# Optimization experiments

Hardware: AMD Instinct MI355X
Metric: run time of the kernel (lower is better)

## Reference

```python
import jax, jax.numpy as jnp
import numpy as np

HEADS = 8
DHEAD = 64
A_SCALE = 8.0  # cosine-attention logit scale (a=8 in source)
ROPE_BASE = 10000.0


def _mp_weight(w, centered):
    # Magnitude-preserving (EDM2-style) weight: optional zero-mean over fan-in,
    # unit-norm per output row, scaled by 1/sqrt(fan_in).
    if centered:
        w = w - w.mean(axis=1, keepdims=True)
    w = w / (jnp.linalg.norm(w, axis=1, keepdims=True) + 1e-8)
    return w / jnp.sqrt(jnp.asarray(w.shape[1], w.dtype))


def _rope_cos_sin(Hs, Ws, d, dtype=jnp.float32):
    # 2D axial RoPE: first d/4 rotation pairs encode row position, last d/4 column position.
    quarter = d // 4
    freqs = 1.0 / (ROPE_BASE ** (jnp.arange(quarter, dtype=dtype) / quarter))  # [d/4]
    ah = jnp.arange(Hs, dtype=dtype)[:, None] * freqs                          # [H, d/4]
    aw = jnp.arange(Ws, dtype=dtype)[:, None] * freqs                          # [W, d/4]
    ang = jnp.concatenate([
        jnp.broadcast_to(ah[:, None, :], (Hs, Ws, quarter)),
        jnp.broadcast_to(aw[None, :, :], (Hs, Ws, quarter)),
    ], axis=-1).reshape(Hs * Ws, d // 2)                                       # [L, d/2]
    return jnp.cos(ang), jnp.sin(ang)


def _apply_rope(t, cos, sin):
    # t: [N, h, L, d]; rotate interleaved pairs.
    x1, x2 = t[..., 0::2], t[..., 1::2]
    r1 = x1 * cos - x2 * sin
    r2 = x1 * sin + x2 * cos
    return jnp.stack([r1, r2], axis=-1).reshape(t.shape)


def setup_inputs() -> dict:
    key = jax.random.key(0)
    ks = jax.random.split(key, 8)
    N, C, Hs, Ws = 8, 256, 32, 32
    E, Hc = 512, 512
    return {
        "x": jax.random.normal(ks[0], (N, C, Hs, Ws), jnp.float32),
        "w": jax.random.normal(ks[1], (N, E), jnp.float32),
        "InputGain": jax.random.uniform(ks[2], (3 * Hc,), jnp.float32),
        "ResidualGain": jax.random.uniform(ks[3], (C,), jnp.float32),
        "qkv_w": jax.random.normal(ks[4], (3 * Hc, C), jnp.float32),
        "qkv_b": jnp.zeros((3 * Hc,), jnp.float32),
        "mod_w": jax.random.normal(ks[5], (E, C), jnp.float32) / jnp.sqrt(512.0),
        "proj_w": jax.random.normal(ks[6], (C, Hc), jnp.float32),
        "sinks": jnp.zeros((HEADS,), jnp.float32),
    }


def reference(x, w, InputGain, ResidualGain, qkv_w, qkv_b, mod_w, proj_w, sinks):
    N, C, Hs, Ws = x.shape
    L = Hs * Ws
    Hc = qkv_w.shape[0] // 3

    # --- fused QKV: style-modulated, biased, centered 1x1 conv with per-out-channel gain ---
    style = w @ mod_w + 1.0                                   # [N, C]
    Wq = _mp_weight(qkv_w, centered=True)                     # [3Hc, C]
    xm = x * style[:, :, None, None]
    y = jnp.einsum('nchw,oc->nohw', xm, Wq)
    y = (y + qkv_b[None, :, None, None]) * InputGain[None, :, None, None]  # [N, 3Hc, H, W]

    # --- split heads, flatten space: [N, h, L, d] ---
    y = y.reshape(N, 3, HEADS, DHEAD, L)
    q = jnp.transpose(y[:, 0], (0, 1, 3, 2))
    k = jnp.transpose(y[:, 1], (0, 1, 3, 2))
    v = jnp.transpose(y[:, 2], (0, 1, 3, 2))

    # --- 2D RoPE on q, k ---
    cos, sin = _rope_cos_sin(Hs, Ws, DHEAD, x.dtype)
    q = _apply_rope(q, cos, sin)
    k = _apply_rope(k, cos, sin)

    # --- cosine attention with per-head sink logit ---
    qn = q / (jnp.linalg.norm(q, axis=-1, keepdims=True) + 1e-8)
    kn = k / (jnp.linalg.norm(k, axis=-1, keepdims=True) + 1e-8)
    logits = A_SCALE * jnp.einsum('nhld,nhmd->nhlm', qn, kn)  # [N, h, L, L]
    sink = jnp.broadcast_to(sinks[None, :, None, None], (N, HEADS, L, 1))
    probs = jax.nn.softmax(jnp.concatenate([logits, sink], axis=-1), axis=-1)[..., :L]
    o = jnp.einsum('nhlm,nhmd->nhld', probs, v)               # [N, h, L, d]

    # --- merge heads back to map, centered 1x1 projection with per-out-channel gain ---
    o = jnp.transpose(o, (0, 1, 3, 2)).reshape(N, Hc, Hs, Ws)
    Wp = _mp_weight(proj_w, centered=True) * ResidualGain[:, None]  # [C, Hc]
    out = jnp.einsum('nchw,oc->nohw', o, Wp)
    return x + out
```

## Files before the change

### kernel.cpp

```cpp
#include <hip/hip_runtime.h>
#include <hip/hip_bf16.h>
#include <math.h>

#define NN 8
#define CC 256
#define LL 1024
#define EE 512
#define HEADS 8
#define DH 64

#define OFF_STYLE   0u
#define OFF_BIAS    2048u
#define OFF_COS     3584u
#define OFF_SIN     36352u
#define OFF_WQB     69120u
#define OFF_WPB     265728u
#define OFF_XMT     331264u
#define OFF_Q       1379840u
#define OFF_K       3476992u
#define OFF_V       5574144u
#define OFF_O       7671296u

typedef __bf16 bf16x8 __attribute__((ext_vector_type(8)));
typedef __bf16 bf16x4 __attribute__((ext_vector_type(4)));
typedef short s16x4 __attribute__((ext_vector_type(4)));
typedef float f32x4 __attribute__((ext_vector_type(4)));

__global__ __launch_bounds__(256) void k_prep(
    const float* __restrict__ w, const float* __restrict__ mod_w, float* __restrict__ style,
    const float* __restrict__ qkv_w, const float* __restrict__ gain,
    const float* __restrict__ bias, __hip_bfloat16* __restrict__ wqb, float* __restrict__ biasg,
    const float* __restrict__ proj_w, const float* __restrict__ rgain,
    __hip_bfloat16* __restrict__ wpb,
    float* __restrict__ cosT, float* __restrict__ sinT) {
    int bid = blockIdx.x;
    int t = threadIdx.x;
    int wv = t >> 6, lane = t & 63;
    if (bid < 384) {
        int o = bid * 4 + wv;
        float4 v = *reinterpret_cast<const float4*>(qkv_w + o * CC + lane * 4);
        float s = v.x + v.y + v.z + v.w;
        #pragma unroll
        for (int off = 1; off < 64; off <<= 1) s += __shfl_xor(s, off);
        float mean = s * (1.0f / 256.0f);
        float c0 = v.x - mean, c1 = v.y - mean, c2 = v.z - mean, c3 = v.w - mean;
        float ss = c0 * c0 + c1 * c1 + c2 * c2 + c3 * c3;
        #pragma unroll
        for (int off = 1; off < 64; off <<= 1) ss += __shfl_xor(ss, off);
        float g = gain[o];
        float scale = g / ((sqrtf(ss) + 1e-8f) * 16.0f);
        bf16x4 outv;
        outv[0] = (__bf16)(c0 * scale); outv[1] = (__bf16)(c1 * scale);
        outv[2] = (__bf16)(c2 * scale); outv[3] = (__bf16)(c3 * scale);
        *reinterpret_cast<bf16x4*>((__bf16*)wqb + o * CC + lane * 4) = outv;
        if (lane == 0) biasg[o] = bias[o] * g;
    } else if (bid < 448) {
        int r = (bid - 384) * 4 + wv;
        const float* p = proj_w + r * 512 + lane * 8;
        float4 v0 = *reinterpret_cast<const float4*>(p);
        float4 v1 = *reinterpret_cast<const float4*>(p + 4);
        float s = v0.x + v0.y + v0.z + v0.w + v1.x + v1.y + v1.z + v1.w;
        #pragma unroll
        for (int off = 1; off < 64; off <<= 1) s += __shfl_xor(s, off);
        float mean = s * (1.0f / 512.0f);
        float c[8] = {v0.x - mean, v0.y - mean, v0.z - mean, v0.w - mean,
                      v1.x - mean, v1.y - mean, v1.z - mean, v1.w - mean};
        float ss = 0.f;
        #pragma unroll
        for (int i = 0; i < 8; ++i) ss += c[i] * c[i];
        #pragma unroll
        for (int off = 1; off < 64; off <<= 1) ss += __shfl_xor(ss, off);
        float scale = rgain[r] / ((sqrtf(ss) + 1e-8f) * 22.62741699796952f);
        bf16x8 outv;
        #pragma unroll
        for (int i = 0; i < 8; ++i) outv[i] = (__bf16)(c[i] * scale);
        *reinterpret_cast<bf16x8*>((__bf16*)wpb + r * 512 + lane * 8) = outv;
    } else if (bid < 512) {
        int idx = (bid - 448) * 256 + t;
        int l = idx >> 4, j = idx & 15;
        int hh = l >> 5, ww = l & 31;
        float f = exp2f(-(float)j * 0.8304820238941836f);
        float s1, c1, s2, c2;
        __sincosf((float)hh * f, &s1, &c1);
        __sincosf((float)ww * f, &s2, &c2);
        cosT[l * 32 + j]      = c1;
        sinT[l * 32 + j]      = s1;
        cosT[l * 32 + 16 + j] = c2;
        sinT[l * 32 + 16 + j] = s2;
    } else {
        int b = bid - 512;
        int n = b >> 2, cg = b & 3;
        int c = cg * 64 + lane;
        __shared__ float red[4][64];
        float acc = 0.f;
        #pragma unroll 8
        for (int e = wv * 128; e < wv * 128 + 128; ++e)
            acc += w[n * EE + e] * mod_w[e * CC + c];
        red[wv][lane] = acc;
        __syncthreads();
        if (wv == 0)
            style[n * CC + c] = red[0][lane] + red[1][lane] + red[2][lane] + red[3][lane] + 1.0f;
    }
}

__global__ __launch_bounds__(256) void k_xm(const float* __restrict__ x,
                                            const float* __restrict__ style,
                                            __hip_bfloat16* __restrict__ xmT) {
    int lb = blockIdx.x;
    int cb = blockIdx.y;
    int n  = blockIdx.z;
    int t = threadIdx.x;
    __shared__ float tile[64][68];
    int r = t >> 2, q = t & 3;
    float st = style[n * CC + cb * 64 + r];
    const float* xp = x + (size_t)n * (CC * LL) + (size_t)(cb * 64 + r) * LL + lb * 64 + q * 16;
    #pragma unroll
    for (int i = 0; i < 4; ++i) {
        float4 v = *reinterpret_cast<const float4*>(xp + i * 4);
        tile[r][q * 16 + i * 4 + 0] = v.x * st;
        tile[r][q * 16 + i * 4 + 1] = v.y * st;
        tile[r][q * 16 + i * 4 + 2] = v.z * st;
        tile[r][q * 16 + i * 4 + 3] = v.w * st;
    }
    __syncthreads();
    __hip_bfloat16 outv[16];
    #pragma unroll
    for (int i = 0; i < 16; ++i)
        outv[i] = __float2bfloat16(tile[q * 16 + i][r]);
    __hip_bfloat16* dst = xmT + (size_t)n * (LL * CC) + (size_t)(lb * 64 + r) * CC + cb * 64 + q * 16;
    *reinterpret_cast<bf16x8*>(dst)     = *reinterpret_cast<bf16x8*>(&outv[0]);
    *reinterpret_cast<bf16x8*>(dst + 8) = *reinterpret_cast<bf16x8*>(&outv[8]);
}

__global__ __launch_bounds__(256) void k_qkv3(const __hip_bfloat16* __restrict__ wqb,
                                              const __hip_bfloat16* __restrict__ xmT,
                                              const float* __restrict__ biasg,
                                              const float* __restrict__ cosT,
                                              const float* __restrict__ sinT,
                                              __hip_bfloat16* __restrict__ qb,
                                              __hip_bfloat16* __restrict__ kb,
                                              __hip_bfloat16* __restrict__ vt) {
    int lb = blockIdx.x;
    int ob = blockIdx.y;
    int n  = blockIdx.z;
    int tid = threadIdx.x;
    int wid = tid >> 6, lane = tid & 63;
    int wr = wid >> 1, wc = wid & 1;
    int g = lane >> 4, r16 = lane & 15;

    int o0 = ob * 128 + wr * 64;
    int l0 = lb * 128 + wc * 64;
    int part = o0 >> 9;
    int h = (o0 & 511) >> 6;

    __shared__ __hip_bfloat16 smem[32768];

    const int srow[4] = {tid >> 3, (tid + 256) >> 3, (tid + 512) >> 3, (tid + 768) >> 3};
    const int scol = (tid & 7) * 8;
    int sswz[4];
    #pragma unroll
    for (int i = 0; i < 4; ++i) sswz[i] = scol ^ ((srow[i] & 7) << 3);

    const __hip_bfloat16* Agl = wqb + (size_t)(ob * 128) * CC;
    const __hip_bfloat16* Bgl = xmT + (size_t)n * (LL * CC) + (size_t)(lb * 128) * CC;

    bf16x8 ar[4], br[4];
    #pragma unroll
    for (int i = 0; i < 4; ++i) {
        ar[i] = *reinterpret_cast<const bf16x8*>(Agl + (size_t)srow[i] * CC + scol);
        br[i] = *reinterpret_cast<const bf16x8*>(Bgl + (size_t)srow[i] * CC + scol);
    }
    #pragma unroll
    for (int i = 0; i < 4; ++i) {
        *reinterpret_cast<bf16x8*>(&smem[srow[i] * 64 + sswz[i]]) = ar[i];
        *reinterpret_cast<bf16x8*>(&smem[16384 + srow[i] * 64 + sswz[i]]) = br[i];
    }
    __syncthreads();

    f32x4 acc[4][4] = {};
    int cur = 0;
    for (int t = 0; t < 4; ++t) {
        if (t < 3) {
            int kt1 = (t + 1) * 64;
            #pragma unroll
            for (int i = 0; i < 4; ++i) {
                ar[i] = *reinterpret_cast<const bf16x8*>(Agl + (size_t)srow[i] * CC + kt1 + scol);
                br[i] = *reinterpret_cast<const bf16x8*>(Bgl + (size_t)srow[i] * CC + kt1 + scol);
            }
        }
        const __hip_bfloat16* At = &smem[cur * 8192];
        const __hip_bfloat16* Bt = &smem[16384 + cur * 8192];
        #pragma unroll
        for (int kk = 0; kk < 2; ++kk) {
            int col = (kk * 32 + g * 8) ^ ((r16 & 7) << 3);
            bf16x8 a[4], b[4];
            #pragma unroll
            for (int m = 0; m < 4; ++m)
                a[m] = *reinterpret_cast<const bf16x8*>(&At[(wr * 64 + m * 16 + r16) * 64 + col]);
            #pragma unroll
            for (int nn = 0; nn < 4; ++nn)
                b[nn] = *reinterpret_cast<const bf16x8*>(&Bt[(wc * 64 + nn * 16 + r16) * 64 + col]);
            __builtin_amdgcn_s_setprio(1);
            #pragma unroll
            for (int m = 0; m < 4; ++m)
                #pragma unroll
                for (int nn = 0; nn < 4; ++nn)
                    acc[m][nn] = __builtin_amdgcn_mfma_f32_16x16x32_bf16(a[m], b[nn], acc[m][nn], 0, 0, 0);
            __builtin_amdgcn_s_setprio(0);
        }
        __syncthreads();
        if (t < 3) {
            #pragma unroll
            for (int i = 0; i < 4; ++i) {
                *reinterpret_cast<bf16x8*>(&smem[(cur ^ 1) * 8192 + srow[i] * 64 + sswz[i]]) = ar[i];
                *reinterpret_cast<bf16x8*>(&smem[16384 + (cur ^ 1) * 8192 + srow[i] * 64 + sswz[i]]) = br[i];
            }
            __syncthreads();
        }
        cur ^= 1;
    }
    __syncthreads();

    __hip_bfloat16 (*sw)[64][72] = reinterpret_cast<__hip_bfloat16 (*)[64][72]>(smem);

    float bg[4][4];
    #pragma unroll
    for (int m = 0; m < 4; ++m)
        #pragma unroll
        for (int reg = 0; reg < 4; ++reg)
            bg[m][reg] = biasg[o0 + m * 16 + 4 * g + reg];

    size_t head = (size_t)(n * 8 + h);

    if (part < 2) {
        __hip_bfloat16* dst = (part == 0) ? qb : kb;
        #pragma unroll
        for (int nn = 0; nn < 4; ++nn) {
            int l = l0 + nn * 16 + r16;
            float rv[4][4];
            float ss = 0.f;
            #pragma unroll
            for (int m = 0; m < 4; ++m) {
                int j0 = m * 8 + g * 2;
                float cA = cosT[l * 32 + j0],     sA = sinT[l * 32 + j0];
                float cB = cosT[l * 32 + j0 + 1], sB = sinT[l * 32 + j0 + 1];
                float x0 = acc[m][nn][0] + bg[m][0];
                float x1 = acc[m][nn][1] + bg[m][1];
                float x2 = acc[m][nn][2] + bg[m][2];
                float x3 = acc[m][nn][3] + bg[m][3];
                rv[m][0] = x0 * cA - x1 * sA;
                rv[m][1] = x0 * sA + x1 * cA;
                rv[m][2] = x2 * cB - x3 * sB;
                rv[m][3] = x2 * sB + x3 * cB;
                ss += rv[m][0] * rv[m][0] + rv[m][1] * rv[m][1] +
                      rv[m][2] * rv[m][2] + rv[m][3] * rv[m][3];
            }
            ss += __shfl_xor(ss, 16);
            ss += __shfl_xor(ss, 32);
            float inv = 1.0f / (sqrtf(ss) + 1e-8f);
            #pragma unroll
            for (int m = 0; m < 4; ++m)
                #pragma unroll
                for (int reg = 0; reg < 4; ++reg)
                    sw[wid][nn * 16 + r16][m * 16 + 4 * g + reg] =
                        __float2bfloat16(rv[m][reg] * inv);
        }
        #pragma unroll
        for (int it = 0; it < 8; ++it) {
            int idx = lane + it * 64;
            int ll = idx >> 3, ch = idx & 7;
            bf16x8 v = *reinterpret_cast<bf16x8*>(&sw[wid][ll][ch * 8]);
            *reinterpret_cast<bf16x8*>(dst + (head * LL + l0 + ll) * DH + ch * 8) = v;
        }
    } else {
        #pragma unroll
        for (int nn = 0; nn < 4; ++nn)
            #pragma unroll
            for (int m = 0; m < 4; ++m)
                #pragma unroll
                for (int reg = 0; reg < 4; ++reg)
                    sw[wid][m * 16 + 4 * g + reg][nn * 16 + r16] =
                        __float2bfloat16(acc[m][nn][reg] + bg[m][reg]);
        #pragma unroll
        for (int it = 0; it < 8; ++it) {
            int idx = lane + it * 64;
            int dd = idx >> 3, ch = idx & 7;
            bf16x8 v = *reinterpret_cast<bf16x8*>(&sw[wid][dd][ch * 8]);
            *reinterpret_cast<bf16x8*>(vt + (head * DH + dd) * LL + l0 + ch * 8) = v;
        }
    }
}

__global__ __launch_bounds__(256) void k_attn_mfma(
    const __hip_bfloat16* __restrict__ qb, const __hip_bfloat16* __restrict__ kb,
    const __hip_bfloat16* __restrict__ vt, const float* __restrict__ sinks,
    __hip_bfloat16* __restrict__ ob) {
    int bid = blockIdx.x;
    int swz = (bid & 7) * 128 + (bid >> 3);
    int n    = swz >> 7;
    int h    = (swz >> 4) & 7;
    int qblk = swz & 15;
    int tid  = threadIdx.x;
    int wid  = tid >> 6, lane = tid & 63;
    int g = lane >> 4, r16 = lane & 15;

    size_t head = (size_t)(n * 8 + h);
    const __hip_bfloat16* Q = qb + head * (size_t)(LL * DH);
    const __hip_bfloat16* K = kb + head * (size_t)(LL * DH);
    const __hip_bfloat16* V = vt + head * (size_t)(DH * LL);
    __hip_bfloat16* O = ob + (size_t)n * (LL * 512) + h * 64;

    int q0 = qblk * 64 + wid * 16;

    __shared__ __hip_bfloat16 kls[2][64][64];
    __shared__ __hip_bfloat16 vls[2][64][64];

    const int cl0 = tid >> 3,        cd0 = (tid & 7) * 8;
    const int cl1 = (tid + 256) >> 3, cd1 = (tid & 7) * 8;
    const int ksw0 = cd0 ^ ((cl0 & 7) << 3);
    const int ksw1 = cd1 ^ ((cl1 & 7) << 3);

    bf16x8 qf[2];
    #pragma unroll
    for (int dc = 0; dc < 2; ++dc)
        qf[dc] = *reinterpret_cast<const bf16x8*>(
            Q + (size_t)(q0 + r16) * DH + dc * 32 + g * 8);

    float snk = sinks[h];
    float m = fmaxf(8.0f, snk);
    const float c1 = 8.0f * 1.44269504f;
    const float c0 = -m * 1.44269504f;

    f32x4 oacc[4];
    #pragma unroll
    for (int dn = 0; dn < 4; ++dn)
        oacc[dn] = (f32x4){0.f, 0.f, 0.f, 0.f};
    f32x4 osum = (f32x4){0.f, 0.f, 0.f, 0.f};
    const s16x4 ones = {(short)0x3F80, (short)0x3F80, (short)0x3F80, (short)0x3F80};

    bf16x8 kr0, kr1, vr0, vr1;
    kr0 = *reinterpret_cast<const bf16x8*>(K + (size_t)cl0 * DH + cd0);
    kr1 = *reinterpret_cast<const bf16x8*>(K + (size_t)cl1 * DH + cd1);
    vr0 = *reinterpret_cast<const bf16x8*>(V + (size_t)cl0 * LL + cd0);
    vr1 = *reinterpret_cast<const bf16x8*>(V + (size_t)cl1 * LL + cd1);
    *reinterpret_cast<bf16x8*>(&kls[0][cl0][ksw0]) = kr0;
    *reinterpret_cast<bf16x8*>(&kls[0][cl1][ksw1]) = kr1;
    *reinterpret_cast<bf16x8*>(&vls[0][cl0][ksw0]) = vr0;
    *reinterpret_cast<bf16x8*>(&vls[0][cl1][ksw1]) = vr1;
    __syncthreads();

    int cur = 0;
    for (int t = 0; t < 16; ++t) {
        if (t < 15) {
            int kt1 = t * 64 + 64;
            kr0 = *reinterpret_cast<const bf16x8*>(K + (size_t)(kt1 + cl0) * DH + cd0);
            kr1 = *reinterpret_cast<const bf16x8*>(K + (size_t)(kt1 + cl1) * DH + cd1);
            vr0 = *reinterpret_cast<const bf16x8*>(V + (size_t)cl0 * LL + kt1 + cd0);
            vr1 = *reinterpret_cast<const bf16x8*>(V + (size_t)cl1 * LL + kt1 + cd1);
        }
        f32x4 sacc[4];
        #pragma unroll
        for (int kn = 0; kn < 4; ++kn)
            sacc[kn] = (f32x4){0.f, 0.f, 0.f, 0.f};
        __builtin_amdgcn_s_setprio(1);
        #pragma unroll
        for (int kn = 0; kn < 4; ++kn) {
            #pragma unroll
            for (int dc = 0; dc < 2; ++dc) {
                bf16x8 kf = *reinterpret_cast<const bf16x8*>(
                    &kls[cur][kn * 16 + r16][(dc * 32 + g * 8) ^ ((r16 & 7) << 3)]);
                sacc[kn] = __builtin_amdgcn_mfma_f32_16x16x32_bf16(
                    kf, qf[dc], sacc[kn], 0, 0, 0);
            }
        }
        __builtin_amdgcn_s_setprio(0);
        #pragma unroll
        for (int kn = 0; kn < 4; ++kn) {
            float p0 = exp2f(fmaf(sacc[kn][0], c1, c0));
            float p1 = exp2f(fmaf(sacc[kn][1], c1, c0));
            float p2 = exp2f(fmaf(sacc[kn][2], c1, c0));
            float p3 = exp2f(fmaf(sacc[kn][3], c1, c0));
            bf16x4 pb;
            pb[0] = (__bf16)p0; pb[1] = (__bf16)p1;
            pb[2] = (__bf16)p2; pb[3] = (__bf16)p3;
            s16x4 pa = __builtin_bit_cast(s16x4, pb);
            __builtin_amdgcn_s_setprio(1);
            osum = __builtin_amdgcn_mfma_f32_16x16x16bf16_1k(pa, ones, osum, 0, 0, 0);
            #pragma unroll
            for (int dn = 0; dn < 4; ++dn) {
                s16x4 vb = *reinterpret_cast<const s16x4*>(
                    &vls[cur][dn * 16 + r16][(kn * 16 + g * 4) ^ ((r16 & 7) << 3)]);
                oacc[dn] = __builtin_amdgcn_mfma_f32_16x16x16bf16_1k(pa, vb, oacc[dn], 0, 0, 0);
            }
            __builtin_amdgcn_s_setprio(0);
        }
        __syncthreads();
        if (t < 15) {
            *reinterpret_cast<bf16x8*>(&kls[cur ^ 1][cl0][ksw0]) = kr0;
            *reinterpret_cast<bf16x8*>(&kls[cur ^ 1][cl1][ksw1]) = kr1;
            *reinterpret_cast<bf16x8*>(&vls[cur ^ 1][cl0][ksw0]) = vr0;
            *reinterpret_cast<bf16x8*>(&vls[cur ^ 1][cl1][ksw1]) = vr1;
            __syncthreads();
        }
        cur ^= 1;
    }

    float sink_e = exp2f((snk - m) * 1.44269504f);
    #pragma unroll
    for (int reg = 0; reg < 4; ++reg) {
        float invq = 1.0f / (osum[reg] + sink_e);
        #pragma unroll
        for (int dn = 0; dn < 4; ++dn)
            O[(size_t)(q0 + 4 * g + reg) * 512 + dn * 16 + r16] =
                __float2bfloat16(oacc[dn][reg] * invq);
    }
}

__global__ __launch_bounds__(256) void k_proj3(const __hip_bfloat16* __restrict__ wpb,
                                               const __hip_bfloat16* __restrict__ ob,
                                               const float* __restrict__ x,
                                               float* __restrict__ out) {
    int lb = blockIdx.x;
    int cb = blockIdx.y;
    int n  = blockIdx.z;
    int tid = threadIdx.x;
    int wid = tid >> 6, lane = tid & 63;
    int wr = wid >> 1, wc = wid & 1;
    int g = lane >> 4, r16 = lane & 15;

    int c0 = cb * 64 + wr * 32;
    int l0 = lb * 128 + wc * 64;

    __shared__ __hip_bfloat16 smem[24576];

    const int arow[2] = {tid >> 3, (tid + 256) >> 3};
    const int brow[4] = {tid >> 3, (tid + 256) >> 3, (tid + 512) >> 3, (tid + 768) >> 3};
    const int scol = (tid & 7) * 8;
    int aswz[2], bswz[4];
    #pragma unroll
    for (int i = 0; i < 2; ++i) aswz[i] = scol ^ ((arow[i] & 7) << 3);
    #pragma unroll
    for (int i = 0; i < 4; ++i) bswz[i] = scol ^ ((brow[i] & 7) << 3);

    const __hip_bfloat16* Agl = wpb + (size_t)(cb * 64) * 512;
    const __hip_bfloat16* Bgl = ob + (size_t)n * (LL * 512) + (size_t)(lb * 128) * 512;

    bf16x8 ar[2], br[4];
    #pragma unroll
    for (int i = 0; i < 2; ++i)
        ar[i] = *reinterpret_cast<const bf16x8*>(Agl + (size_t)arow[i] * 512 + scol);
    #pragma unroll
    for (int i = 0; i < 4; ++i)
        br[i] = *reinterpret_cast<const bf16x8*>(Bgl + (size_t)brow[i] * 512 + scol);
    #pragma unroll
    for (int i = 0; i < 2; ++i)
        *reinterpret_cast<bf16x8*>(&smem[arow[i] * 64 + aswz[i]]) = ar[i];
    #pragma unroll
    for (int i = 0; i < 4; ++i)
        *reinterpret_cast<bf16x8*>(&smem[8192 + brow[i] * 64 + bswz[i]]) = br[i];
    __syncthreads();

    f32x4 acc[2][4] = {};
    int cur = 0;
    for (int t = 0; t < 8; ++t) {
        if (t < 7) {
            int kt1 = (t + 1) * 64;
            #pragma unroll
            for (int i = 0; i < 2; ++i)
                ar[i] = *reinterpret_cast<const bf16x8*>(Agl + (size_t)arow[i] * 512 + kt1 + scol);
            #pragma unroll
            for (int i = 0; i < 4; ++i)
                br[i] = *reinterpret_cast<const bf16x8*>(Bgl + (size_t)brow[i] * 512 + kt1 + scol);
        }
        const __hip_bfloat16* At = &smem[cur * 4096];
        const __hip_bfloat16* Bt = &smem[8192 + cur * 8192];
        #pragma unroll
        for (int kk = 0; kk < 2; ++kk) {
            int col = (kk * 32 + g * 8) ^ ((r16 & 7) << 3);
            bf16x8 a[2], b[4];
            #pragma unroll
            for (int m = 0; m < 2; ++m)
                a[m] = *reinterpret_cast<const bf16x8*>(&At[(wr * 32 + m * 16 + r16) * 64 + col]);
            #pragma unroll
            for (int nn = 0; nn < 4; ++nn)
                b[nn] = *reinterpret_cast<const bf16x8*>(&Bt[(wc * 64 + nn * 16 + r16) * 64 + col]);
            __builtin_amdgcn_s_setprio(1);
            #pragma unroll
            for (int m = 0; m < 2; ++m)
                #pragma unroll
                for (int nn = 0; nn < 4; ++nn)
                    acc[m][nn] = __builtin_amdgcn_mfma_f32_16x16x32_bf16(a[m], b[nn], acc[m][nn], 0, 0, 0);
            __builtin_amdgcn_s_setprio(0);
        }
        __syncthreads();
        if (t < 7) {
            #pragma unroll
            for (int i = 0; i < 2; ++i)
                *reinterpret_cast<bf16x8*>(&smem[(cur ^ 1) * 4096 + arow[i] * 64 + aswz[i]]) = ar[i];
            #pragma unroll
            for (int i = 0; i < 4; ++i)
                *reinterpret_cast<bf16x8*>(&smem[8192 + (cur ^ 1) * 8192 + brow[i] * 64 + bswz[i]]) = br[i];
            __syncthreads();
        }
        cur ^= 1;
    }

    #pragma unroll
    for (int m = 0; m < 2; ++m) {
        #pragma unroll
        for (int reg = 0; reg < 4; ++reg) {
            int c = c0 + m * 16 + 4 * g + reg;
            #pragma unroll
            for (int nn = 0; nn < 4; ++nn) {
                int l = l0 + nn * 16 + r16;
                size_t idx = (size_t)n * (CC * LL) + (size_t)c * LL + l;
                out[idx] = x[idx] + acc[m][nn][reg];
            }
        }
    }
}

extern "C" void kernel_launch(void* const* d_in, const int* in_sizes, int n_in,
                              void* d_out, int out_size, void* d_ws, size_t ws_size,
                              hipStream_t stream) {
    const float* x       = (const float*)d_in[0];
    const float* w       = (const float*)d_in[1];
    const float* igain   = (const float*)d_in[2];
    const float* rgain   = (const float*)d_in[3];
    const float* qkv_w   = (const float*)d_in[4];
    const float* qkv_b   = (const float*)d_in[5];
    const float* mod_w   = (const float*)d_in[6];
    const float* proj_w  = (const float*)d_in[7];
    const float* sinks   = (const float*)d_in[8];
    float* out = (float*)d_out;
    float* ws  = (float*)d_ws;

    float* style = ws + OFF_STYLE;
    float* biasg = ws + OFF_BIAS;
    float* cosT  = ws + OFF_COS;
    float* sinT  = ws + OFF_SIN;
    __hip_bfloat16* wqb = (__hip_bfloat16*)(ws + OFF_WQB);
    __hip_bfloat16* wpb = (__hip_bfloat16*)(ws + OFF_WPB);
    __hip_bfloat16* xmT = (__hip_bfloat16*)(ws + OFF_XMT);
    __hip_bfloat16* qb  = (__hip_bfloat16*)(ws + OFF_Q);
    __hip_bfloat16* kb  = (__hip_bfloat16*)(ws + OFF_K);
    __hip_bfloat16* vt  = (__hip_bfloat16*)(ws + OFF_V);
    __hip_bfloat16* obuf = (__hip_bfloat16*)(ws + OFF_O);

    k_prep<<<544, 256, 0, stream>>>(w, mod_w, style, qkv_w, igain, qkv_b, wqb, biasg,
                                    proj_w, rgain, wpb, cosT, sinT);
    k_xm<<<dim3(16, 4, NN), 256, 0, stream>>>(x, style, xmT);
    k_qkv3<<<dim3(8, 12, NN), 256, 0, stream>>>(wqb, xmT, biasg, cosT, sinT, qb, kb, vt);
    k_attn_mfma<<<1024, 256, 0, stream>>>(qb, kb, vt, sinks, obuf);
    k_proj3<<<dim3(8, 4, NN), 256, 0, stream>>>(wpb, obuf, x, out);
}
```

Baseline: 85.55 us.

## Drop redundant barriers in double-buffered loops and reswizzle V tile in LDS

In all three double-buffered GEMM/attention loops, the barrier before writing the next buffer is removed, leaving one barrier per iteration after the store. This works because the write goes to the other buffer, which was last read in the previous iteration. In the attention kernel, the V tile now uses a 4-element XOR swizzle keyed on (row&15), and stores are split into two 8-byte writes. This is meant to cut LDS bank conflicts on the 4-wide V fragment reads. The cost is more LDS store instructions and reliance on the reasoning that one barrier per iteration is enough.

```diff
diff --git a/kernel.cpp b/kernel.cpp
--- a/kernel.cpp
+++ b/kernel.cpp
@@ -24,6 +24,7 @@
 typedef __bf16 bf16x8 __attribute__((ext_vector_type(8)));
 typedef __bf16 bf16x4 __attribute__((ext_vector_type(4)));
 typedef short s16x4 __attribute__((ext_vector_type(4)));
+typedef short s16x8 __attribute__((ext_vector_type(8)));
 typedef float f32x4 __attribute__((ext_vector_type(4)));
 
 __global__ __launch_bounds__(256) void k_prep(
@@ -208,18 +209,16 @@
                     acc[m][nn] = __builtin_amdgcn_mfma_f32_16x16x32_bf16(a[m], b[nn], acc[m][nn], 0, 0, 0);
             __builtin_amdgcn_s_setprio(0);
         }
-        __syncthreads();
         if (t < 3) {
             #pragma unroll
             for (int i = 0; i < 4; ++i) {
                 *reinterpret_cast<bf16x8*>(&smem[(cur ^ 1) * 8192 + srow[i] * 64 + sswz[i]]) = ar[i];
                 *reinterpret_cast<bf16x8*>(&smem[16384 + (cur ^ 1) * 8192 + srow[i] * 64 + sswz[i]]) = br[i];
             }
-            __syncthreads();
-        }
+        }
+        __syncthreads();
         cur ^= 1;
     }
-    __syncthreads();
 
     __hip_bfloat16 (*sw)[64][72] = reinterpret_cast<__hip_bfloat16 (*)[64][72]>(smem);
 
@@ -315,10 +314,14 @@
     __shared__ __hip_bfloat16 kls[2][64][64];
     __shared__ __hip_bfloat16 vls[2][64][64];
 
-    const int cl0 = tid >> 3,        cd0 = (tid & 7) * 8;
-    const int cl1 = (tid + 256) >> 3, cd1 = (tid & 7) * 8;
+    const int cl0 = tid >> 3,         cd0 = (tid & 7) * 8;
+    const int cl1 = (tid + 256) >> 3;
     const int ksw0 = cd0 ^ ((cl0 & 7) << 3);
-    const int ksw1 = cd1 ^ ((cl1 & 7) << 3);
+    const int ksw1 = cd0 ^ ((cl1 & 7) << 3);
+    const int vswA0 = cd0       ^ ((cl0 & 15) << 2);
+    const int vswB0 = (cd0 + 4) ^ ((cl0 & 15) << 2);
+    const int vswA1 = cd0       ^ ((cl1 & 15) << 2);
+    const int vswB1 = (cd0 + 4) ^ ((cl1 & 15) << 2);
 
     bf16x8 qf[2];
     #pragma unroll
@@ -340,13 +343,19 @@
 
     bf16x8 kr0, kr1, vr0, vr1;
     kr0 = *reinterpret_cast<const bf16x8*>(K + (size_t)cl0 * DH + cd0);
-    kr1 = *reinterpret_cast<const bf16x8*>(K + (size_t)cl1 * DH + cd1);
+    kr1 = *reinterpret_cast<const bf16x8*>(K + (size_t)cl1 * DH + cd0);
     vr0 = *reinterpret_cast<const bf16x8*>(V + (size_t)cl0 * LL + cd0);
-    vr1 = *reinterpret_cast<const bf16x8*>(V + (size_t)cl1 * LL + cd1);
-    *reinterpret_cast<bf16x8*>(&kls[0][cl0][ksw0]) = kr0;
-    *reinterpret_cast<bf16x8*>(&kls[0][cl1][ksw1]) = kr1;
-    *reinterpret_cast<bf16x8*>(&vls[0][cl0][ksw0]) = vr0;
-    *reinterpret_cast<bf16x8*>(&vls[0][cl1][ksw1]) = vr1;
+    vr1 = *reinterpret_cast<const bf16x8*>(V + (size_t)cl1 * LL + cd0);
+    {
+        *reinterpret_cast<bf16x8*>(&kls[0][cl0][ksw0]) = kr0;
+        *reinterpret_cast<bf16x8*>(&kls[0][cl1][ksw1]) = kr1;
+        s16x8 w0 = __builtin_bit_cast(s16x8, vr0);
+        s16x8 w1 = __builtin_bit_cast(s16x8, vr1);
+        *reinterpret_cast<s16x4*>(&vls[0][cl0][vswA0]) = __builtin_shufflevector(w0, w0, 0, 1, 2, 3);
+        *reinterpret_cast<s16x4*>(&vls[0][cl0][vswB0]) = __builtin_shufflevector(w0, w0, 4, 5, 6, 7);
+        *reinterpret_cast<s16x4*>(&vls[0][cl1][vswA1]) = __builtin_shufflevector(w1, w1, 0, 1, 2, 3);
+        *reinterpret_cast<s16x4*>(&vls[0][cl1][vswB1]) = __builtin_shufflevector(w1, w1, 4, 5, 6, 7);
+    }
     __syncthreads();
 
     int cur = 0;
@@ -354,9 +363,9 @@
         if (t < 15) {
             int kt1 = t * 64 + 64;
             kr0 = *reinterpret_cast<const bf16x8*>(K + (size_t)(kt1 + cl0) * DH + cd0);
-            kr1 = *reinterpret_cast<const bf16x8*>(K + (size_t)(kt1 + cl1) * DH + cd1);
+            kr1 = *reinterpret_cast<const bf16x8*>(K + (size_t)(kt1 + cl1) * DH + cd0);
             vr0 = *reinterpret_cast<const bf16x8*>(V + (size_t)cl0 * LL + kt1 + cd0);
-            vr1 = *reinterpret_cast<const bf16x8*>(V + (size_t)cl1 * LL + kt1 + cd1);
+            vr1 = *reinterpret_cast<const bf16x8*>(V + (size_t)cl1 * LL + kt1 + cd0);
         }
         f32x4 sacc[4];
         #pragma unroll
@@ -389,19 +398,22 @@
             #pragma unroll
             for (int dn = 0; dn < 4; ++dn) {
                 s16x4 vb = *reinterpret_cast<const s16x4*>(
-                    &vls[cur][dn * 16 + r16][(kn * 16 + g * 4) ^ ((r16 & 7) << 3)]);
+                    &vls[cur][dn * 16 + r16][(kn * 16 + g * 4) ^ ((r16 & 15) << 2)]);
                 oacc[dn] = __builtin_amdgcn_mfma_f32_16x16x16bf16_1k(pa, vb, oacc[dn], 0, 0, 0);
             }
             __builtin_amdgcn_s_setprio(0);
         }
-        __syncthreads();
         if (t < 15) {
             *reinterpret_cast<bf16x8*>(&kls[cur ^ 1][cl0][ksw0]) = kr0;
             *reinterpret_cast<bf16x8*>(&kls[cur ^ 1][cl1][ksw1]) = kr1;
-            *reinterpret_cast<bf16x8*>(&vls[cur ^ 1][cl0][ksw0]) = vr0;
-            *reinterpret_cast<bf16x8*>(&vls[cur ^ 1][cl1][ksw1]) = vr1;
-            __syncthreads();
-        }
+            s16x8 w0 = __builtin_bit_cast(s16x8, vr0);
+            s16x8 w1 = __builtin_bit_cast(s16x8, vr1);
+            *reinterpret_cast<s16x4*>(&vls[cur ^ 1][cl0][vswA0]) = __builtin_shufflevector(w0, w0, 0, 1, 2, 3);
+            *reinterpret_cast<s16x4*>(&vls[cur ^ 1][cl0][vswB0]) = __builtin_shufflevector(w0, w0, 4, 5, 6, 7);
+            *reinterpret_cast<s16x4*>(&vls[cur ^ 1][cl1][vswA1]) = __builtin_shufflevector(w1, w1, 0, 1, 2, 3);
+            *reinterpret_cast<s16x4*>(&vls[cur ^ 1][cl1][vswB1]) = __builtin_shufflevector(w1, w1, 4, 5, 6, 7);
+        }
+        __syncthreads();
         cur ^= 1;
     }
 
@@ -492,7 +504,6 @@
                     acc[m][nn] = __builtin_amdgcn_mfma_f32_16x16x32_bf16(a[m], b[nn], acc[m][nn], 0, 0, 0);
             __builtin_amdgcn_s_setprio(0);
         }
-        __syncthreads();
         if (t < 7) {
             #pragma unroll
             for (int i = 0; i < 2; ++i)
@@ -500,8 +511,8 @@
             #pragma unroll
             for (int i = 0; i < 4; ++i)
                 *reinterpret_cast<bf16x8*>(&smem[8192 + (cur ^ 1) * 8192 + brow[i] * 64 + bswz[i]]) = br[i];
-            __syncthreads();
-        }
+        }
+        __syncthreads();
         cur ^= 1;
     }
 
```

Measured after the change: 85.22 us. About the same (-0.4%).
